# Performance work log

Measured on AMD Instinct MI355X. Metric: run time of the kernel, lower is better.

The kernel has to match this reference:

```python
import jax, jax.numpy as jnp
import numpy as np

B, S = 128, 128
AH, VH, TH = 64, 64, 128  # audio/vision/text LSTM hidden sizes
FUSED = (AH + 1) * (VH + 1) * (TH + 1)  # 545025
PF = 128  # post_fusion_dim


def setup_inputs() -> dict:
    key = jax.random.key(0)
    ks = jax.random.split(key, 6)
    return {
        "audio_h": jax.random.normal(ks[0], (B, S, AH), jnp.float32),
        "vision_h": jax.random.normal(ks[1], (B, S, VH), jnp.float32),
        "text_h": jax.random.normal(ks[2], (B, S, TH), jnp.float32),
        "W1": jax.random.normal(ks[3], (PF, FUSED), jnp.float32) * 0.001,
        "b1": jnp.zeros((PF,), jnp.float32),
        "W2": jax.random.normal(ks[4], (PF, PF), jnp.float32) * 0.05,
        "b2": jnp.zeros((PF,), jnp.float32),
        "W3": jax.random.normal(ks[5], (1, PF), jnp.float32) * 0.05,
        "b3": jnp.zeros((1,), jnp.float32),
    }


def reference(audio_h, vision_h, text_h, W1, b1, W2, b2, W3, b3):
    b, s = audio_h.shape[0], audio_h.shape[1]
    ones = jnp.ones((b, s, 1), audio_h.dtype)
    a = jnp.concatenate([ones, audio_h], axis=2)   # [B,S,AH+1]
    v = jnp.concatenate([ones, vision_h], axis=2)  # [B,S,VH+1]
    t = jnp.concatenate([ones, text_h], axis=2)    # [B,S,TH+1]
    # sum_t outer(a_t, v_t, t_t): one fused contraction over the time axis
    fusion = jnp.einsum('bsa,bsv,bsw->bavw', a, v, t)  # [B,AH+1,VH+1,TH+1]
    fusion = fusion.reshape(b, -1)                      # matches torch view order (a,v,t)
    # T2FN low-rank regularizer scale
    tmp = jnp.sqrt(jnp.asarray(AH * VH * TH / max(AH, VH, TH), jnp.float32))
    # post-fusion MLP (dropout p=0 -> identity)
    y1 = jax.nn.relu(fusion @ W1.T + b1)
    y2 = jax.nn.relu(y1 @ W2.T + b2)
    out = y2 @ W3.T + b3  # [B,1]
    out = jax.nn.sigmoid(out) * 6.0 - 3.0  # output_range=6, output_shift=-3
    norm = jnp.linalg.norm(fusion, axis=1)  # [B]
    reg_loss = jnp.mean(tmp * norm)
    return (out, reg_loss)
```

## Files before the change

kernel.cpp:

```cpp
#include <hip/hip_runtime.h>
#include <math.h>

#define BB 128
#define SS 128
#define AE 65
#define VE 65
#define TE 129
#define PFD 128
#define FUSED 545025UL
#define FUSEDI 545025
#define VSTRIDE 136
#define APLANE 8840
#define FPP 574976UL
#define FPPI 574976
#define KSP 512
#define NBLK 1123

typedef _Float16 half8 __attribute__((ext_vector_type(8)));
typedef float f32x16 __attribute__((ext_vector_type(16)));

__device__ __forceinline__ void gll16(const void* g, void* l) {
  __builtin_amdgcn_global_load_lds((const __attribute__((address_space(1))) void*)g,
                                   (__attribute__((address_space(3))) void*)l, 16, 0, 0);
}

__global__ __launch_bounds__(256) void k_initf(_Float16* __restrict__ Fh,
                                               float* __restrict__ y1pre,
                                               float* __restrict__ normsq,
                                               float* __restrict__ Flast) {
  const int b = blockIdx.x;
  const int tid = threadIdx.x;
  _Float16* base = Fh + (size_t)b * FPP;
  for (int i = tid; i < 29575; i += 256) {
    const int a = i / 455, r = i - a * 455;
    const int v = r / 7, e = r - v * 7;
    base[a * APLANE + v * VSTRIDE + 129 + e] = (_Float16)0.f;
  }
  for (int i = tid; i < 376; i += 256) base[574600 + i] = (_Float16)0.f;
  if (tid < PFD) y1pre[b * PFD + tid] = 0.f;
  if (tid == 128) normsq[b] = 0.f;
  if (tid == 129) Flast[b] = 0.f;
}

__global__ __launch_bounds__(256) void k_core(
    const float* __restrict__ audio, const float* __restrict__ vision,
    const float* __restrict__ text, _Float16* __restrict__ Fh,
    float* __restrict__ normsq)
{
  const int b  = blockIdx.x;
  const int gy = blockIdx.y;
  const int gz = blockIdx.z;
  const int tid = threadIdx.x;
  const int wv = tid >> 6, ln = tid & 63;
  const int lr = ln & 31, hb = ln >> 5;

  __shared__ float    sVt[64][132];
  __shared__ float    sAc[8][132];
  __shared__ _Float16 sTh[64][136];
  __shared__ _Float16 sTl[64][136];

  {
    const float* vb = vision + (size_t)b * SS * 64;
#pragma unroll
    for (int r = 0; r < 32; ++r) {
      const int e = tid + 256 * r;
      sVt[e & 63][e >> 6] = vb[e];
    }
    const float* ab = audio + (size_t)b * SS * 64 + 8 * gy;
#pragma unroll
    for (int r = 0; r < 4; ++r) {
      const int e = tid + 256 * r;
      sAc[e & 7][e >> 3] = ab[(e >> 3) * 64 + (e & 7)];
    }
    const int wbase = 64 * gz;
    const float* tb = text + (size_t)b * SS * 128;
#pragma unroll
    for (int r = 0; r < 32; ++r) {
      const int e = tid + 256 * r;
      const int s = e >> 6, wl = e & 63;
      const int w = wbase + wl;
      const float val = (w == 0) ? 1.f : tb[s * 128 + w - 1];
      const _Float16 th = (_Float16)val;
      sTh[wl][s] = th;
      sTl[wl][s] = (_Float16)((val - (float)th) * 2048.f);
    }
  }
  __syncthreads();

  float ss = 0.f;
  for (int i = 0; i < 8; ++i) {
    const int u  = 8 * wv + i;
    const int rt = u >> 1, wt = u & 1;
    const int j  = rt >> 1, vh = rt & 1;
    const int v0m = 32 * vh;
    const int wl0 = 32 * wt;

    f32x16 acc = {}, accl = {};
#pragma unroll
    for (int ks = 0; ks < 8; ++ks) {
      const int s0 = 16 * ks + 8 * hb;
      const float4 x0 = *(const float4*)&sVt[v0m + lr][s0];
      const float4 x1 = *(const float4*)&sVt[v0m + lr][s0 + 4];
      const float4 a0 = *(const float4*)&sAc[j][s0];
      const float4 a1 = *(const float4*)&sAc[j][s0 + 4];
      const float pp[8] = {a0.x * x0.x, a0.y * x0.y, a0.z * x0.z, a0.w * x0.w,
                           a1.x * x1.x, a1.y * x1.y, a1.z * x1.z, a1.w * x1.w};
      half8 afh, afl;
#pragma unroll
      for (int e = 0; e < 8; ++e) {
        const _Float16 h = (_Float16)pp[e];
        afh[e] = h;
        afl[e] = (_Float16)((pp[e] - (float)h) * 2048.f);
      }
      const half8 bqh = *(const half8*)&sTh[wl0 + lr][s0];
      const half8 bql = *(const half8*)&sTl[wl0 + lr][s0];
      acc  = __builtin_amdgcn_mfma_f32_32x32x16_f16(afh, bqh, acc,  0, 0, 0);
      accl = __builtin_amdgcn_mfma_f32_32x32x16_f16(afl, bqh, accl, 0, 0, 0);
      accl = __builtin_amdgcn_mfma_f32_32x32x16_f16(afh, bql, accl, 0, 0, 0);
    }

    const int a = 1 + 8 * gy + j;
    _Float16* Fb = Fh + (size_t)b * FPP + (size_t)a * APLANE;
    const int wg = 64 * gz + wl0 + lr;
#pragma unroll
    for (int reg = 0; reg < 16; ++reg) {
      const int crow = (reg & 3) + 8 * (reg >> 2) + 4 * hb;
      const int v = 1 + 32 * vh + crow;
      const float f = acc[reg] + accl[reg] * (1.f / 2048.f);
      ss += f * f;
      Fb[(size_t)v * VSTRIDE + wg] = (_Float16)f;
    }
  }

#pragma unroll
  for (int off = 32; off > 0; off >>= 1) ss += __shfl_down(ss, off);
  if (ln == 0) atomicAdd(&normsq[b], ss);
}

__global__ __launch_bounds__(256) void k_planes(
    const float* __restrict__ audio, const float* __restrict__ vision,
    const float* __restrict__ text, _Float16* __restrict__ Fh,
    float* __restrict__ Flast, float* __restrict__ normsq)
{
  const int b = blockIdx.x;
  const int which = blockIdx.y;
  const int tid = threadIdx.x;
  const int tw = tid & 15, tv = tid >> 4;
  __shared__ __align__(16) char smem[28800];

  float ss = 0.f;

  if (which == 0) {
    float (*sv)[80]  = (float(*)[80])smem;
    float (*st)[144] = (float(*)[144])(smem + 10240);
    float acc[5][9];
#pragma unroll
    for (int i = 0; i < 5; ++i)
#pragma unroll
      for (int j = 0; j < 9; ++j) acc[i][j] = 0.f;

    for (int c = 0; c < 4; ++c) {
      const int s0 = 32 * c;
      __syncthreads();
      const float* vbase = &vision[((size_t)(b * SS + s0)) * 64];
#pragma unroll
      for (int r = 0; r < 8; ++r) {
        const int e = tid + 256 * r;
        sv[e >> 6][(e & 63) + 1] = vbase[e];
      }
      const float* tbase = &text[((size_t)(b * SS + s0)) * 128];
#pragma unroll
      for (int r = 0; r < 16; ++r) {
        const int e = tid + 256 * r;
        st[e >> 7][(e & 127) + 1] = tbase[e];
      }
      if (tid < 32) { sv[tid][0] = 1.f; st[tid][0] = 1.f; }
      __syncthreads();
      for (int s = 0; s < 32; ++s) {
        float vr[5], tr[9];
#pragma unroll
        for (int i = 0; i < 5; ++i) {
          const int vx = tv + 16 * i;
          vr[i] = (vx < VE) ? sv[s][vx] : 0.f;
        }
#pragma unroll
        for (int j = 0; j < 9; ++j) {
          const int wx = tw + 16 * j;
          tr[j] = (wx < TE) ? st[s][wx] : 0.f;
        }
#pragma unroll
        for (int i = 0; i < 5; ++i)
#pragma unroll
          for (int j = 0; j < 9; ++j) acc[i][j] += vr[i] * tr[j];
      }
    }
    _Float16* Fb = Fh + (size_t)b * FPP;
#pragma unroll
    for (int i = 0; i < 5; ++i) {
      const int v = tv + 16 * i;
      if (v < VE) {
#pragma unroll
        for (int j = 0; j < 9; ++j) {
          const int w = tw + 16 * j;
          if (w < TE) {
            const float m = acc[i][j];
            Fb[(size_t)v * VSTRIDE + w] = (_Float16)m;
            ss += m * m;
          }
        }
      }
    }
  } else if (which == 1) {
    float (*sa)[64]  = (float(*)[64])smem;
    float (*st)[144] = (float(*)[144])(smem + 10240);
    float acc[4][9];
#pragma unroll
    for (int i = 0; i < 4; ++i)
#pragma unroll
      for (int j = 0; j < 9; ++j) acc[i][j] = 0.f;

    for (int c = 0; c < 4; ++c) {
      const int s0 = 32 * c;
      __syncthreads();
      const float* abase = &audio[((size_t)(b * SS + s0)) * 64];
#pragma unroll
      for (int r = 0; r < 8; ++r) {
        const int e = tid + 256 * r;
        sa[e >> 6][e & 63] = abase[e];
      }
      const float* tbase = &text[((size_t)(b * SS + s0)) * 128];
#pragma unroll
      for (int r = 0; r < 16; ++r) {
        const int e = tid + 256 * r;
        st[e >> 7][(e & 127) + 1] = tbase[e];
      }
      if (tid < 32) st[tid][0] = 1.f;
      __syncthreads();
      for (int s = 0; s < 32; ++s) {
        float ar[4], tr[9];
#pragma unroll
        for (int i = 0; i < 4; ++i) ar[i] = sa[s][tv + 16 * i];
#pragma unroll
        for (int j = 0; j < 9; ++j) {
          const int wx = tw + 16 * j;
          tr[j] = (wx < TE) ? st[s][wx] : 0.f;
        }
#pragma unroll
        for (int i = 0; i < 4; ++i)
#pragma unroll
          for (int j = 0; j < 9; ++j) acc[i][j] += ar[i] * tr[j];
      }
    }
#pragma unroll
    for (int i = 0; i < 4; ++i) {
      const int a = 1 + tv + 16 * i;
      _Float16* Fb = Fh + (size_t)b * FPP + (size_t)a * APLANE;
#pragma unroll
      for (int j = 0; j < 9; ++j) {
        const int w = tw + 16 * j;
        if (w < TE) {
          const float m = acc[i][j];
          Fb[w] = (_Float16)m;
          ss += m * m;
        }
      }
    }
  } else {
    float (*sa)[64] = (float(*)[64])smem;
    float (*sv)[64] = (float(*)[64])(smem + 10240);
    float* swt = (float*)(smem + 10240 + 8192);
    float acc[4][4];
#pragma unroll
    for (int i = 0; i < 4; ++i)
#pragma unroll
      for (int j = 0; j < 4; ++j) acc[i][j] = 0.f;

    for (int c = 0; c < 4; ++c) {
      const int s0 = 32 * c;
      __syncthreads();
      const float* abase = &audio[((size_t)(b * SS + s0)) * 64];
      const float* vbase = &vision[((size_t)(b * SS + s0)) * 64];
#pragma unroll
      for (int r = 0; r < 8; ++r) {
        const int e = tid + 256 * r;
        sa[e >> 6][e & 63] = abase[e];
        sv[e >> 6][e & 63] = vbase[e];
      }
      if (tid < 32) swt[tid] = text[((size_t)(b * SS + s0 + tid)) * 128 + 127];
      __syncthreads();
      for (int s = 0; s < 32; ++s) {
        const float t = swt[s];
        float ar[4], vr[4];
#pragma unroll
        for (int i = 0; i < 4; ++i) ar[i] = sa[s][tv + 16 * i] * t;
#pragma unroll
        for (int j = 0; j < 4; ++j) vr[j] = sv[s][tw + 16 * j];
#pragma unroll
        for (int i = 0; i < 4; ++i)
#pragma unroll
          for (int j = 0; j < 4; ++j) acc[i][j] += ar[i] * vr[j];
      }
    }
#pragma unroll
    for (int i = 0; i < 4; ++i) {
      const int a = 1 + tv + 16 * i;
      _Float16* Fb = Fh + (size_t)b * FPP + (size_t)a * APLANE;
#pragma unroll
      for (int j = 0; j < 4; ++j) {
        const int v = 1 + tw + 16 * j;
        float m = acc[i][j];
        ss += m * m;
        if (a == 64 && v == 64) { Flast[b] = m; m = 0.f; }
        Fb[(size_t)v * VSTRIDE + 128] = (_Float16)m;
      }
    }
  }

#pragma unroll
  for (int off = 32; off > 0; off >>= 1) ss += __shfl_down(ss, off);
  if ((tid & 63) == 0) atomicAdd(&normsq[b], ss);
}

__global__ __launch_bounds__(256) void k_gemm(
    const float* __restrict__ W1, const _Float16* __restrict__ Fh,
    float* __restrict__ parts)
{
  __shared__ _Float16 sB[3][4096];

  const int tid = threadIdx.x;
  const int wv = tid >> 6, ln = tid & 63;
  const int lb = ln & 31, hb = ln >> 5;
  const int p  = (wv << 5) + lb;
  const int kp0 = blockIdx.x * KSP;
  const int kpl0 = kp0 + (hb << 3);
  const int kpl1 = kpl0 + 16;

  int w0, ko0, w1, ko1;
  {
    const int a0 = kpl0 / APLANE; const int r0 = kpl0 - a0 * APLANE;
    const int v0 = r0 / VSTRIDE;  w0 = r0 - v0 * VSTRIDE;
    ko0 = a0 * 8385 + v0 * 129 + w0;
    const int a1 = kpl1 / APLANE; const int r1 = kpl1 - a1 * APLANE;
    const int v1 = r1 / VSTRIDE;  w1 = r1 - v1 * VSTRIDE;
    ko1 = a1 * 8385 + v1 * 129 + w1;
  }

  const float* wrow = W1 + (size_t)p * FUSED;

  const int brow0 = (wv << 5) + (ln >> 2);
  const int slogB = (ln & 3) ^ ((ln >> 2) & 3);
  const _Float16* FhP0 = Fh + (size_t)brow0 * FPP + kp0 + (slogB << 3);
  const _Float16* FhP1 = FhP0 + (size_t)16 * FPP;

  f32x16 acc0 = {}, acc1 = {}, acc2 = {}, acc3 = {};
  float4 xaP[4], xaQ[4];

#define LOADA(S)                                                           \
  {                                                                        \
    const int kc0 = (ko0 <= 545017) ? ko0 : 545008;                        \
    const int kc1 = (ko1 <= 545017) ? ko1 : 545008;                        \
    __builtin_memcpy(&xa##S[0], wrow + kc0, 16);                           \
    __builtin_memcpy(&xa##S[1], wrow + kc0 + 4, 16);                       \
    __builtin_memcpy(&xa##S[2], wrow + kc1, 16);                           \
    __builtin_memcpy(&xa##S[3], wrow + kc1 + 4, 16);                       \
    w0 += 32; if (w0 >= VSTRIDE) { w0 -= VSTRIDE; ko0 += 25; } else ko0 += 32; \
    w1 += 32; if (w1 >= VSTRIDE) { w1 -= VSTRIDE; ko1 += 25; } else ko1 += 32; \
  }

#define STAGEB(BUF, KOFF)                                                 \
  {                                                                       \
    gll16(FhP0 + (KOFF), (char*)&sB[BUF][0] + ((wv << 5) << 6));          \
    gll16(FhP1 + (KOFF), (char*)&sB[BUF][0] + (((wv << 5) + 16) << 6));   \
  }

#define GSTEP(T, S, WSTR)                                                      \
  {                                                                            \
    asm volatile("s_waitcnt " WSTR ::: "memory");                              \
    __builtin_amdgcn_sched_barrier(0);                                         \
    __builtin_amdgcn_s_barrier();                                              \
    __builtin_amdgcn_sched_barrier(0);                                         \
    half8 af0, af1;                                                            \
    af0[0] = (_Float16)xa##S[0].x; af0[1] = (_Float16)xa##S[0].y;              \
    af0[2] = (_Float16)xa##S[0].z; af0[3] = (_Float16)xa##S[0].w;              \
    af0[4] = (_Float16)xa##S[1].x; af0[5] = (_Float16)xa##S[1].y;              \
    af0[6] = (_Float16)xa##S[1].z; af0[7] = (_Float16)xa##S[1].w;              \
    af1[0] = (_Float16)xa##S[2].x; af1[1] = (_Float16)xa##S[2].y;              \
    af1[2] = (_Float16)xa##S[2].z; af1[3] = (_Float16)xa##S[2].w;              \
    af1[4] = (_Float16)xa##S[3].x; af1[5] = (_Float16)xa##S[3].y;              \
    af1[6] = (_Float16)xa##S[3].z; af1[7] = (_Float16)xa##S[3].w;              \
    if ((T) + 2 < 16) { LOADA(S) STAGEB(((T) + 2) % 3, ((T) + 2) * 32) }       \
    __builtin_amdgcn_sched_barrier(0);                                         \
    {                                                                          \
      const _Float16* sBb = &sB[(T) % 3][0];                                   \
      {                                                                        \
        const int sl = hb;                                                     \
        const char* bbase = (const char*)sBb + (lb << 6) + ((sl ^ (lb & 3)) << 4); \
        const half8 b0 = *(const half8*)(bbase);                               \
        const half8 b1 = *(const half8*)(bbase + 2048);                        \
        const half8 b2 = *(const half8*)(bbase + 4096);                        \
        const half8 b3 = *(const half8*)(bbase + 6144);                        \
        acc0 = __builtin_amdgcn_mfma_f32_32x32x16_f16(af0, b0, acc0, 0, 0, 0); \
        acc1 = __builtin_amdgcn_mfma_f32_32x32x16_f16(af0, b1, acc1, 0, 0, 0); \
        acc2 = __builtin_amdgcn_mfma_f32_32x32x16_f16(af0, b2, acc2, 0, 0, 0); \
        acc3 = __builtin_amdgcn_mfma_f32_32x32x16_f16(af0, b3, acc3, 0, 0, 0); \
      }                                                                        \
      {                                                                        \
        const int sl = 2 + hb;                                                 \
        const char* bbase = (const char*)sBb + (lb << 6) + ((sl ^ (lb & 3)) << 4); \
        const half8 b0 = *(const half8*)(bbase);                               \
        const half8 b1 = *(const half8*)(bbase + 2048);                        \
        const half8 b2 = *(const half8*)(bbase + 4096);                        \
        const half8 b3 = *(const half8*)(bbase + 6144);                        \
        acc0 = __builtin_amdgcn_mfma_f32_32x32x16_f16(af1, b0, acc0, 0, 0, 0); \
        acc1 = __builtin_amdgcn_mfma_f32_32x32x16_f16(af1, b1, acc1, 0, 0, 0); \
        acc2 = __builtin_amdgcn_mfma_f32_32x32x16_f16(af1, b2, acc2, 0, 0, 0); \
        acc3 = __builtin_amdgcn_mfma_f32_32x32x16_f16(af1, b3, acc3, 0, 0, 0); \
      }                                                                        \
    }                                                                          \
  }

  LOADA(P)
  STAGEB(0, 0)
  LOADA(Q)
  STAGEB(1, 32)

  GSTEP(0,  P, "vmcnt(6)")
  GSTEP(1,  Q, "vmcnt(6)")
  GSTEP(2,  P, "vmcnt(6)")
  GSTEP(3,  Q, "vmcnt(6)")
  GSTEP(4,  P, "vmcnt(6)")
  GSTEP(5,  Q, "vmcnt(6)")
  GSTEP(6,  P, "vmcnt(6)")
  GSTEP(7,  Q, "vmcnt(6)")
  GSTEP(8,  P, "vmcnt(6)")
  GSTEP(9,  Q, "vmcnt(6)")
  GSTEP(10, P, "vmcnt(6)")
  GSTEP(11, Q, "vmcnt(6)")
  GSTEP(12, P, "vmcnt(6)")
  GSTEP(13, Q, "vmcnt(6)")
  GSTEP(14, P, "vmcnt(6)")
  GSTEP(15, Q, "vmcnt(0)")
#undef GSTEP
#undef LOADA
#undef STAGEB

  f32x16* o = (f32x16*)(parts + ((size_t)blockIdx.x * 256 + tid) * 64);
  o[0] = acc0; o[1] = acc1; o[2] = acc2; o[3] = acc3;
}

__global__ __launch_bounds__(256) void k_red(const float* __restrict__ parts,
                                             float* __restrict__ y1pre)
{
  const int tid = threadIdx.x;
  const int T = blockIdx.x * 4 + (tid >> 6);
  const int R = tid & 63;
  float s = 0.f;
  for (int sl = blockIdx.y; sl < NBLK; sl += 16)
    s += parts[(size_t)sl * 16384 + T * 64 + R];
  const int wv2 = T >> 6, hb2 = (T >> 5) & 1, lb2 = T & 31;
  const int q = R >> 4, rg = R & 15;
  const int b = q * 32 + lb2;
  const int pp = wv2 * 32 + (rg & 3) + 8 * (rg >> 2) + 4 * hb2;
  atomicAdd(&y1pre[b * PFD + pp], s);
}

__global__ __launch_bounds__(128) void k_final(
    const float* __restrict__ y1pre, const float* __restrict__ b1,
    const float* __restrict__ W2, const float* __restrict__ b2,
    const float* __restrict__ W3, const float* __restrict__ b3,
    const float* __restrict__ W1, const float* __restrict__ Flast,
    const float* __restrict__ normsq, float* __restrict__ out)
{
  const int b = blockIdx.x, p = threadIdx.x;
  __shared__ float y1[PFD];
  __shared__ float red[PFD];
  const float extra = W1[(size_t)p * FUSED + (FUSED - 1)] * Flast[b];
  y1[p] = fmaxf(y1pre[(size_t)b * PFD + p] + extra + b1[p], 0.f);
  __syncthreads();
  float s = b2[p];
  for (int k = 0; k < PFD; ++k) s += y1[k] * W2[p * PFD + k];
  const float y2 = fmaxf(s, 0.f);
  red[p] = y2 * W3[p];
  __syncthreads();
  for (int off = 64; off > 0; off >>= 1) {
    if (p < off) red[p] += red[p + off];
    __syncthreads();
  }
  if (p == 0) {
    const float x = red[0] + b3[0];
    out[b] = 6.f / (1.f + expf(-x)) - 3.f;
  }
  if (b == 0) {
    __syncthreads();
    red[p] = sqrtf(normsq[p]);
    __syncthreads();
    for (int off = 64; off > 0; off >>= 1) {
      if (p < off) red[p] += red[p + off];
      __syncthreads();
    }
    if (p == 0) out[BB] = 64.f * red[0] / (float)BB;
  }
}

extern "C" void kernel_launch(void* const* d_in, const int* in_sizes, int n_in,
                              void* d_out, int out_size, void* d_ws, size_t ws_size,
                              hipStream_t stream) {
  const float* audio  = (const float*)d_in[0];
  const float* vision = (const float*)d_in[1];
  const float* text   = (const float*)d_in[2];
  const float* W1     = (const float*)d_in[3];
  const float* b1     = (const float*)d_in[4];
  const float* W2     = (const float*)d_in[5];
  const float* b2     = (const float*)d_in[6];
  const float* W3     = (const float*)d_in[7];
  const float* b3     = (const float*)d_in[8];
  float* out = (float*)d_out;

  float* y1pre  = (float*)d_ws;
  float* normsq = y1pre + BB * PFD;
  float* Flast  = normsq + BB;
  _Float16* Fh  = (_Float16*)((char*)d_ws + 131072);
  float* parts  = (float*)((char*)d_ws + 147324928);

  k_initf<<<BB, 256, 0, stream>>>(Fh, y1pre, normsq, Flast);

  k_core<<<dim3(BB, 8, 2), 256, 0, stream>>>(audio, vision, text, Fh, normsq);
  k_planes<<<dim3(BB, 3), 256, 0, stream>>>(audio, vision, text, Fh, Flast, normsq);

  k_gemm<<<NBLK, 256, 0, stream>>>(W1, Fh, parts);
  k_red<<<dim3(64, 16), 256, 0, stream>>>(parts, y1pre);

  k_final<<<BB, PFD, 0, stream>>>(y1pre, b1, W2, b2, W3, b3, W1, Flast, normsq, out);
}
```

Before: 335.3 us.

## Widen GEMM k-step to 64 with double buffering and share A-fragments in fusion kernel

The W1 GEMM's pipeline moves from 16 steps of k=32 with a triple-buffered LDS ring and hand-placed waitcnts to 8 steps of k=64. It uses two 16KB LDS buffers, an 8-slot XOR swizzle and a __syncthreads per step, which cuts barrier count and loop overhead per k. Separately, the fusion kernel computes both 32-wide text halves per A/V fragment, so the product and hi/lo split are reused across twice the MFMAs. The trade-off is the loss of the explicit vmcnt-based prefetch depth: the loads issued for step t+1 are only one stage ahead, which may expose memory latency. Register pressure also rises in both kernels.

```diff
diff --git a/kernel.cpp b/kernel.cpp
--- a/kernel.cpp
+++ b/kernel.cpp
@@ -15,6 +15,7 @@
 #define FPPI 574976
 #define KSP 512
 #define NBLK 1123
+#define NST 8
 
 typedef _Float16 half8 __attribute__((ext_vector_type(8)));
 typedef float f32x16 __attribute__((ext_vector_type(16)));
@@ -88,14 +89,12 @@
   __syncthreads();
 
   float ss = 0.f;
-  for (int i = 0; i < 8; ++i) {
-    const int u  = 8 * wv + i;
-    const int rt = u >> 1, wt = u & 1;
+  for (int r = 0; r < 4; ++r) {
+    const int rt = 4 * wv + r;
     const int j  = rt >> 1, vh = rt & 1;
     const int v0m = 32 * vh;
-    const int wl0 = 32 * wt;
-
-    f32x16 acc = {}, accl = {};
+
+    f32x16 accA = {}, acclA = {}, accB = {}, acclB = {};
 #pragma unroll
     for (int ks = 0; ks < 8; ++ks) {
       const int s0 = 16 * ks + 8 * hb;
@@ -112,23 +111,31 @@
         afh[e] = h;
         afl[e] = (_Float16)((pp[e] - (float)h) * 2048.f);
       }
-      const half8 bqh = *(const half8*)&sTh[wl0 + lr][s0];
-      const half8 bql = *(const half8*)&sTl[wl0 + lr][s0];
-      acc  = __builtin_amdgcn_mfma_f32_32x32x16_f16(afh, bqh, acc,  0, 0, 0);
-      accl = __builtin_amdgcn_mfma_f32_32x32x16_f16(afl, bqh, accl, 0, 0, 0);
-      accl = __builtin_amdgcn_mfma_f32_32x32x16_f16(afh, bql, accl, 0, 0, 0);
+      const half8 bqh0 = *(const half8*)&sTh[lr][s0];
+      const half8 bql0 = *(const half8*)&sTl[lr][s0];
+      const half8 bqh1 = *(const half8*)&sTh[32 + lr][s0];
+      const half8 bql1 = *(const half8*)&sTl[32 + lr][s0];
+      accA  = __builtin_amdgcn_mfma_f32_32x32x16_f16(afh, bqh0, accA,  0, 0, 0);
+      acclA = __builtin_amdgcn_mfma_f32_32x32x16_f16(afl, bqh0, acclA, 0, 0, 0);
+      acclA = __builtin_amdgcn_mfma_f32_32x32x16_f16(afh, bql0, acclA, 0, 0, 0);
+      accB  = __builtin_amdgcn_mfma_f32_32x32x16_f16(afh, bqh1, accB,  0, 0, 0);
+      acclB = __builtin_amdgcn_mfma_f32_32x32x16_f16(afl, bqh1, acclB, 0, 0, 0);
+      acclB = __builtin_amdgcn_mfma_f32_32x32x16_f16(afh, bql1, acclB, 0, 0, 0);
     }
 
     const int a = 1 + 8 * gy + j;
     _Float16* Fb = Fh + (size_t)b * FPP + (size_t)a * APLANE;
-    const int wg = 64 * gz + wl0 + lr;
+    const int wg0 = 64 * gz + lr;
+    const int wg1 = 64 * gz + 32 + lr;
 #pragma unroll
     for (int reg = 0; reg < 16; ++reg) {
       const int crow = (reg & 3) + 8 * (reg >> 2) + 4 * hb;
       const int v = 1 + 32 * vh + crow;
-      const float f = acc[reg] + accl[reg] * (1.f / 2048.f);
-      ss += f * f;
-      Fb[(size_t)v * VSTRIDE + wg] = (_Float16)f;
+      const float fA = accA[reg] + acclA[reg] * (1.f / 2048.f);
+      const float fB = accB[reg] + acclB[reg] * (1.f / 2048.f);
+      ss += fA * fA + fB * fB;
+      Fb[(size_t)v * VSTRIDE + wg0] = (_Float16)fA;
+      Fb[(size_t)v * VSTRIDE + wg1] = (_Float16)fB;
     }
   }
 
@@ -325,122 +332,90 @@
     const float* __restrict__ W1, const _Float16* __restrict__ Fh,
     float* __restrict__ parts)
 {
-  __shared__ _Float16 sB[3][4096];
+  __shared__ _Float16 sB[2][8192];
 
   const int tid = threadIdx.x;
   const int wv = tid >> 6, ln = tid & 63;
   const int lb = ln & 31, hb = ln >> 5;
   const int p  = (wv << 5) + lb;
   const int kp0 = blockIdx.x * KSP;
-  const int kpl0 = kp0 + (hb << 3);
-  const int kpl1 = kpl0 + 16;
-
-  int w0, ko0, w1, ko1;
-  {
-    const int a0 = kpl0 / APLANE; const int r0 = kpl0 - a0 * APLANE;
-    const int v0 = r0 / VSTRIDE;  w0 = r0 - v0 * VSTRIDE;
-    ko0 = a0 * 8385 + v0 * 129 + w0;
-    const int a1 = kpl1 / APLANE; const int r1 = kpl1 - a1 * APLANE;
-    const int v1 = r1 / VSTRIDE;  w1 = r1 - v1 * VSTRIDE;
-    ko1 = a1 * 8385 + v1 * 129 + w1;
-  }
-
+
+  int wtr[4], kot[4];
+#pragma unroll
+  for (int j = 0; j < 4; ++j) {
+    const int kpl = kp0 + 16 * j + (hb << 3);
+    const int a = kpl / APLANE;
+    const int rem = kpl - a * APLANE;
+    const int v = rem / VSTRIDE;
+    wtr[j] = rem - v * VSTRIDE;
+    kot[j] = a * 8385 + v * 129 + wtr[j];
+  }
   const float* wrow = W1 + (size_t)p * FUSED;
 
-  const int brow0 = (wv << 5) + (ln >> 2);
-  const int slogB = (ln & 3) ^ ((ln >> 2) & 3);
-  const _Float16* FhP0 = Fh + (size_t)brow0 * FPP + kp0 + (slogB << 3);
-  const _Float16* FhP1 = FhP0 + (size_t)16 * FPP;
+  const int brow = (wv << 5) + (ln >> 3);
+  const int sslot = (ln & 7) ^ ((ln >> 3) & 7);
+  const _Float16* FhB = Fh + (size_t)brow * FPP + kp0 + (sslot << 3);
 
   f32x16 acc0 = {}, acc1 = {}, acc2 = {}, acc3 = {};
-  float4 xaP[4], xaQ[4];
-
-#define LOADA(S)                                                           \
+  float4 xa[8];
+
+#define LOADA                                                              \
   {                                                                        \
-    const int kc0 = (ko0 <= 545017) ? ko0 : 545008;                        \
-    const int kc1 = (ko1 <= 545017) ? ko1 : 545008;                        \
-    __builtin_memcpy(&xa##S[0], wrow + kc0, 16);                           \
-    __builtin_memcpy(&xa##S[1], wrow + kc0 + 4, 16);                       \
-    __builtin_memcpy(&xa##S[2], wrow + kc1, 16);                           \
-    __builtin_memcpy(&xa##S[3], wrow + kc1 + 4, 16);                       \
-    w0 += 32; if (w0 >= VSTRIDE) { w0 -= VSTRIDE; ko0 += 25; } else ko0 += 32; \
-    w1 += 32; if (w1 >= VSTRIDE) { w1 -= VSTRIDE; ko1 += 25; } else ko1 += 32; \
-  }
-
-#define STAGEB(BUF, KOFF)                                                 \
-  {                                                                       \
-    gll16(FhP0 + (KOFF), (char*)&sB[BUF][0] + ((wv << 5) << 6));          \
-    gll16(FhP1 + (KOFF), (char*)&sB[BUF][0] + (((wv << 5) + 16) << 6));   \
-  }
-
-#define GSTEP(T, S, WSTR)                                                      \
-  {                                                                            \
-    asm volatile("s_waitcnt " WSTR ::: "memory");                              \
-    __builtin_amdgcn_sched_barrier(0);                                         \
-    __builtin_amdgcn_s_barrier();                                              \
-    __builtin_amdgcn_sched_barrier(0);                                         \
-    half8 af0, af1;                                                            \
-    af0[0] = (_Float16)xa##S[0].x; af0[1] = (_Float16)xa##S[0].y;              \
-    af0[2] = (_Float16)xa##S[0].z; af0[3] = (_Float16)xa##S[0].w;              \
-    af0[4] = (_Float16)xa##S[1].x; af0[5] = (_Float16)xa##S[1].y;              \
-    af0[6] = (_Float16)xa##S[1].z; af0[7] = (_Float16)xa##S[1].w;              \
-    af1[0] = (_Float16)xa##S[2].x; af1[1] = (_Float16)xa##S[2].y;              \
-    af1[2] = (_Float16)xa##S[2].z; af1[3] = (_Float16)xa##S[2].w;              \
-    af1[4] = (_Float16)xa##S[3].x; af1[5] = (_Float16)xa##S[3].y;              \
-    af1[6] = (_Float16)xa##S[3].z; af1[7] = (_Float16)xa##S[3].w;              \
-    if ((T) + 2 < 16) { LOADA(S) STAGEB(((T) + 2) % 3, ((T) + 2) * 32) }       \
-    __builtin_amdgcn_sched_barrier(0);                                         \
-    {                                                                          \
-      const _Float16* sBb = &sB[(T) % 3][0];                                   \
-      {                                                                        \
-        const int sl = hb;                                                     \
-        const char* bbase = (const char*)sBb + (lb << 6) + ((sl ^ (lb & 3)) << 4); \
-        const half8 b0 = *(const half8*)(bbase);                               \
-        const half8 b1 = *(const half8*)(bbase + 2048);                        \
-        const half8 b2 = *(const half8*)(bbase + 4096);                        \
-        const half8 b3 = *(const half8*)(bbase + 6144);                        \
-        acc0 = __builtin_amdgcn_mfma_f32_32x32x16_f16(af0, b0, acc0, 0, 0, 0); \
-        acc1 = __builtin_amdgcn_mfma_f32_32x32x16_f16(af0, b1, acc1, 0, 0, 0); \
-        acc2 = __builtin_amdgcn_mfma_f32_32x32x16_f16(af0, b2, acc2, 0, 0, 0); \
-        acc3 = __builtin_amdgcn_mfma_f32_32x32x16_f16(af0, b3, acc3, 0, 0, 0); \
-      }                                                                        \
-      {                                                                        \
-        const int sl = 2 + hb;                                                 \
-        const char* bbase = (const char*)sBb + (lb << 6) + ((sl ^ (lb & 3)) << 4); \
-        const half8 b0 = *(const half8*)(bbase);                               \
-        const half8 b1 = *(const half8*)(bbase + 2048);                        \
-        const half8 b2 = *(const half8*)(bbase + 4096);                        \
-        const half8 b3 = *(const half8*)(bbase + 6144);                        \
-        acc0 = __builtin_amdgcn_mfma_f32_32x32x16_f16(af1, b0, acc0, 0, 0, 0); \
-        acc1 = __builtin_amdgcn_mfma_f32_32x32x16_f16(af1, b1, acc1, 0, 0, 0); \
-        acc2 = __builtin_amdgcn_mfma_f32_32x32x16_f16(af1, b2, acc2, 0, 0, 0); \
-        acc3 = __builtin_amdgcn_mfma_f32_32x32x16_f16(af1, b3, acc3, 0, 0, 0); \
-      }                                                                        \
-    }                                                                          \
-  }
-
-  LOADA(P)
+    _Pragma("unroll")                                                      \
+    for (int j = 0; j < 4; ++j) {                                          \
+      const int kc = (kot[j] <= 545017) ? kot[j] : 545008;                 \
+      __builtin_memcpy(&xa[2 * j], wrow + kc, 16);                         \
+      __builtin_memcpy(&xa[2 * j + 1], wrow + kc + 4, 16);                 \
+      wtr[j] += 64;                                                        \
+      if (wtr[j] >= VSTRIDE) { wtr[j] -= VSTRIDE; kot[j] += 57; }          \
+      else kot[j] += 64;                                                   \
+    }                                                                      \
+  }
+
+#define STAGEB(BUF, KOFF)                                                  \
+  {                                                                        \
+    _Pragma("unroll")                                                      \
+    for (int n = 0; n < 4; ++n) {                                          \
+      gll16(FhB + (size_t)(n << 3) * FPP + (KOFF),                         \
+            (char*)&sB[BUF][0] + (((wv << 5) + (n << 3)) << 7));           \
+    }                                                                      \
+  }
+
+  LOADA
   STAGEB(0, 0)
-  LOADA(Q)
-  STAGEB(1, 32)
-
-  GSTEP(0,  P, "vmcnt(6)")
-  GSTEP(1,  Q, "vmcnt(6)")
-  GSTEP(2,  P, "vmcnt(6)")
-  GSTEP(3,  Q, "vmcnt(6)")
-  GSTEP(4,  P, "vmcnt(6)")
-  GSTEP(5,  Q, "vmcnt(6)")
-  GSTEP(6,  P, "vmcnt(6)")
-  GSTEP(7,  Q, "vmcnt(6)")
-  GSTEP(8,  P, "vmcnt(6)")
-  GSTEP(9,  Q, "vmcnt(6)")
-  GSTEP(10, P, "vmcnt(6)")
-  GSTEP(11, Q, "vmcnt(6)")
-  GSTEP(12, P, "vmcnt(6)")
-  GSTEP(13, Q, "vmcnt(6)")
-  GSTEP(14, P, "vmcnt(6)")
-  GSTEP(15, Q, "vmcnt(0)")
-#undef GSTEP
+  __syncthreads();
+
+  int buf = 0;
+  for (int t = 0; t < NST; ++t) {
+    half8 af[4];
+#pragma unroll
+    for (int j = 0; j < 4; ++j) {
+      af[j][0] = (_Float16)xa[2 * j].x;     af[j][1] = (_Float16)xa[2 * j].y;
+      af[j][2] = (_Float16)xa[2 * j].z;     af[j][3] = (_Float16)xa[2 * j].w;
+      af[j][4] = (_Float16)xa[2 * j + 1].x; af[j][5] = (_Float16)xa[2 * j + 1].y;
+      af[j][6] = (_Float16)xa[2 * j + 1].z; af[j][7] = (_Float16)xa[2 * j + 1].w;
+    }
+    if (t + 1 < NST) {
+      LOADA
+      STAGEB(buf ^ 1, (t + 1) * 64)
+    }
+    const _Float16* sBb = &sB[buf][0];
+#pragma unroll
+    for (int j = 0; j < 4; ++j) {
+      const int slot = ((j << 1) + hb) ^ (lb & 7);
+      const char* bbase = (const char*)sBb + (lb << 7) + (slot << 4);
+      const half8 b0 = *(const half8*)(bbase);
+      const half8 b1 = *(const half8*)(bbase + 4096);
+      const half8 b2 = *(const half8*)(bbase + 8192);
+      const half8 b3 = *(const half8*)(bbase + 12288);
+      acc0 = __builtin_amdgcn_mfma_f32_32x32x16_f16(af[j], b0, acc0, 0, 0, 0);
+      acc1 = __builtin_amdgcn_mfma_f32_32x32x16_f16(af[j], b1, acc1, 0, 0, 0);
+      acc2 = __builtin_amdgcn_mfma_f32_32x32x16_f16(af[j], b2, acc2, 0, 0, 0);
+      acc3 = __builtin_amdgcn_mfma_f32_32x32x16_f16(af[j], b3, acc3, 0, 0, 0);
+    }
+    __syncthreads();
+    buf ^= 1;
+  }
 #undef LOADA
 #undef STAGEB
 
```

New measurement: 350.5 us. 1.05x slower.
